# Performance work log

Measured on AMD Instinct MI355X. Metric: run time of the kernel, lower is better.

## Reference

```python
import jax, jax.numpy as jnp
import numpy as np

B, S, D, H = 2, 2048, 1024, 16
DK = D // H  # 64


def setup_inputs() -> dict:
    key = jax.random.key(0)
    ks = jax.random.split(key, 9)
    query = jax.random.normal(ks[0], (B, S, D), dtype=jnp.float32)
    k_in = jax.random.normal(ks[1], (B, S, D), dtype=jnp.float32)
    v_in = jax.random.normal(ks[2], (B, S, D), dtype=jnp.float32)
    mask = jax.random.randint(ks[3], (B, S, S), 0, 2, dtype=jnp.int32)
    sc = 1.0 / np.sqrt(D)
    Wq = jax.random.normal(ks[4], (H, D, DK), dtype=jnp.float32) * sc  # per-head q proj
    Wk = jax.random.normal(ks[5], (H, D, DK), dtype=jnp.float32) * sc
    Wv = jax.random.normal(ks[6], (H, D, DK), dtype=jnp.float32) * sc
    Wu = jax.random.normal(ks[7], (D, D), dtype=jnp.float32) * sc  # unifyheads weight
    bu = jax.random.normal(ks[8], (D,), dtype=jnp.float32) * 0.01
    return {"query": query, "key": k_in, "value": v_in, "mask": mask,
            "Wq": Wq, "Wk": Wk, "Wv": Wv, "Wu": Wu, "bu": bu}


def reference(query, key, value, mask, Wq, Wk, Wv, Wu, bu):
    scale = DK ** 0.25  # original divides q and k each by d_k^(1/4)
    q = jnp.einsum('bsd,hdk->bhsk', query, Wq) / scale
    k = jnp.einsum('bsd,hdk->bhsk', key, Wk) / scale
    v = jnp.einsum('bsd,hdk->bhsk', value, Wv)
    scores = jnp.einsum('bhsk,bhtk->bhst', q, k)  # [B,H,S,S]
    scores = jnp.where(mask[:, None, :, :] == 0, jnp.float32(-1e9), scores)
    attn = jax.nn.softmax(scores, axis=-1)
    out = jnp.einsum('bhst,bhtk->bhsk', attn, v)
    out = jnp.transpose(out, (0, 2, 1, 3)).reshape(query.shape[0], query.shape[1], D)  # concat heads
    return out @ Wu + bu
```

## Files before the change

### kernel.cpp

```cpp
#include <hip/hip_runtime.h>
#include <hip/hip_bf16.h>


typedef __bf16 bf16_t;
typedef __attribute__((ext_vector_type(4))) __bf16 bf16x4;
typedef __attribute__((ext_vector_type(8))) __bf16 bf16x8;
typedef __attribute__((ext_vector_type(4))) float f32x4;
typedef unsigned int u32;

#define B_ 2
#define S_ 2048
#define D_ 1024
#define H_ 16
#define DK_ 64
#define NX_ (4096 * 1024)

static __device__ __forceinline__ f32x4 mfma16(bf16x8 a, bf16x8 b, f32x4 c) {
  return __builtin_amdgcn_mfma_f32_16x16x32_bf16(a, b, c, 0, 0, 0);
}

static __device__ __forceinline__ void async16(const bf16_t* g, bf16_t* l) {
  __builtin_amdgcn_global_load_lds(
      (const __attribute__((address_space(1))) u32*)g,
      (__attribute__((address_space(3))) u32*)l, 16, 0, 0);
}

__global__ __launch_bounds__(256) void cvt_x(const float* __restrict__ q,
                                             const float* __restrict__ k,
                                             const float* __restrict__ v,
                                             bf16_t* __restrict__ qo,
                                             bf16_t* __restrict__ ko,
                                             bf16_t* __restrict__ vo) {
  const int z = blockIdx.y;
  const float* src = (z == 0) ? q : (z == 1) ? k : v;
  bf16_t* dst = (z == 0) ? qo : (z == 1) ? ko : vo;
  size_t i = ((size_t)blockIdx.x * 256 + threadIdx.x) * 8;
  float4 a = *(const float4*)(src + i);
  float4 b = *(const float4*)(src + i + 4);
  bf16x8 o;
  o[0] = (bf16_t)a.x; o[1] = (bf16_t)a.y; o[2] = (bf16_t)a.z; o[3] = (bf16_t)a.w;
  o[4] = (bf16_t)b.x; o[5] = (bf16_t)b.y; o[6] = (bf16_t)b.z; o[7] = (bf16_t)b.w;
  *(bf16x8*)(dst + i) = o;
}

__global__ __launch_bounds__(256) void wtrans(
    const float* __restrict__ Wq, const float* __restrict__ Wk,
    const float* __restrict__ Wv, const float* __restrict__ Wu,
    bf16_t* __restrict__ Bq, bf16_t* __restrict__ Bk,
    bf16_t* __restrict__ Bv, bf16_t* __restrict__ Bu, float qkscale) {
  __shared__ __align__(16) bf16_t T[64][72];
  const int z = blockIdx.z;
  const float* W = (z == 0) ? Wq : (z == 1) ? Wk : (z == 2) ? Wv : Wu;
  bf16_t* BT = (z == 0) ? Bq : (z == 1) ? Bk : (z == 2) ? Bv : Bu;
  const float scale = (z <= 1) ? qkscale : 1.0f;
  const int d0 = blockIdx.x * 64, nt = blockIdx.y;
  const int tid = threadIdx.x;
  const int r = tid & 63, g = tid >> 6;

  const float* src = (z < 3)
      ? W + ((size_t)nt * D_ + d0 + r) * DK_ + g * 16
      : W + (size_t)(d0 + r) * D_ + nt * 64 + g * 16;
#pragma unroll
  for (int j = 0; j < 4; ++j) {
    float4 w4 = *(const float4*)(src + j * 4);
    T[g * 16 + j * 4 + 0][r] = (bf16_t)(w4.x * scale);
    T[g * 16 + j * 4 + 1][r] = (bf16_t)(w4.y * scale);
    T[g * 16 + j * 4 + 2][r] = (bf16_t)(w4.z * scale);
    T[g * 16 + j * 4 + 3][r] = (bf16_t)(w4.w * scale);
  }
  __syncthreads();
  const int orow = tid >> 3, seg = tid & 7;
#pragma unroll
  for (int p = 0; p < 2; ++p) {
    int rr = p * 32 + orow;
    *(bf16x8*)(BT + (size_t)(nt * 64 + rr) * D_ + d0 + seg * 8) =
        *(const bf16x8*)&T[rr][seg * 8];
  }
}

__global__ __launch_bounds__(256) void vt_build(const bf16_t* __restrict__ V,
                                                bf16_t* __restrict__ Vt) {
  __shared__ __align__(16) bf16_t T[64][72];
  const int r0 = blockIdx.x * 64;
  const int c0 = blockIdx.y * 64;
  const int tid = threadIdx.x;
#pragma unroll
  for (int it = 0; it < 2; ++it) {
    int t = tid + it * 256;
    int rr = t >> 3, cc = (t & 7) * 8;
    *(bf16x8*)&T[rr][cc] = *(const bf16x8*)(V + (size_t)(r0 + rr) * D_ + c0 + cc);
  }
  __syncthreads();
#pragma unroll
  for (int it = 0; it < 2; ++it) {
    int t = tid + it * 256;
    int cr = t >> 3, rc = (t & 7) * 8;
    bf16x8 v;
#pragma unroll
    for (int j = 0; j < 8; ++j) v[j] = T[rc + j][cr];
    *(bf16x8*)(Vt + (size_t)(c0 + cr) * 4096 + r0 + rc) = v;
  }
}

__global__ __launch_bounds__(256) void mask_pack(const int* __restrict__ mask,
                                                 unsigned int* __restrict__ bits) {
  int w = blockIdx.x * 256 + threadIdx.x;
  const int4* p = (const int4*)(mask + (size_t)w * 32);
  unsigned int v = 0;
#pragma unroll
  for (int i = 0; i < 8; ++i) {
    int4 m4 = p[i];
    v |= (m4.x != 0 ? 1u : 0u) << (i * 4 + 0);
    v |= (m4.y != 0 ? 1u : 0u) << (i * 4 + 1);
    v |= (m4.z != 0 ? 1u : 0u) << (i * 4 + 2);
    v |= (m4.w != 0 ? 1u : 0u) << (i * 4 + 3);
  }
  bits[w] = v;
}

__global__ __launch_bounds__(256) void gemm_bt(
    const bf16_t* __restrict__ A0, const bf16_t* __restrict__ A1,
    const bf16_t* __restrict__ A2, const bf16_t* __restrict__ BT0,
    const bf16_t* __restrict__ BT1, const bf16_t* __restrict__ BT2,
    bf16_t* __restrict__ C0, bf16_t* __restrict__ C1, bf16_t* __restrict__ C2) {
  __shared__ __align__(16) bf16_t As[128 * 64];
  __shared__ __align__(16) bf16_t Bs[128 * 64];

  const int z = blockIdx.z;
  const bf16_t* A = (z == 0) ? A0 : (z == 1) ? A1 : A2;
  const bf16_t* BT = (z == 0) ? BT0 : (z == 1) ? BT1 : BT2;
  bf16_t* C = (z == 0) ? C0 : (z == 1) ? C1 : C2;

  const int tid = threadIdx.x;
  const int lane = tid & 63, wave = tid >> 6;
  const int l = lane & 15, quad = lane >> 4;
  const int wm = wave >> 1, wn = wave & 1;
  const int row0 = blockIdx.x * 128, col0 = blockIdx.y * 128;

  const int lr = lane >> 3;
  const int gc8 = (lane & 7) ^ lr;
  const int xl = l & 7;

  f32x4 acc[4][4];
#pragma unroll
  for (int i = 0; i < 4; ++i)
#pragma unroll
    for (int j = 0; j < 4; ++j) acc[i][j] = {0.f, 0.f, 0.f, 0.f};

  for (int k0 = 0; k0 < 1024; k0 += 64) {
    __syncthreads();
#pragma unroll
    for (int c = 0; c < 4; ++c) {
      int r = wave * 32 + c * 8;
      async16(A + (size_t)(row0 + r + lr) * 1024 + k0 + gc8 * 8, As + r * 64);
      async16(BT + (size_t)(col0 + r + lr) * 1024 + k0 + gc8 * 8, Bs + r * 64);
    }
    __syncthreads();

#pragma unroll
    for (int kh = 0; kh < 2; ++kh) {
      bf16x8 af[4], bf[4];
#pragma unroll
      for (int f = 0; f < 4; ++f)
        af[f] = *(const bf16x8*)&As[(wm * 64 + f * 16 + l) * 64 +
                                    (((kh * 4 + quad) ^ xl) * 8)];
#pragma unroll
      for (int f = 0; f < 4; ++f)
        bf[f] = *(const bf16x8*)&Bs[(wn * 64 + f * 16 + l) * 64 +
                                    (((kh * 4 + quad) ^ xl) * 8)];
#pragma unroll
      for (int fm = 0; fm < 4; ++fm)
#pragma unroll
        for (int fn = 0; fn < 4; ++fn)
          acc[fm][fn] = mfma16(af[fm], bf[fn], acc[fm][fn]);
    }
  }

#pragma unroll
  for (int fm = 0; fm < 4; ++fm)
#pragma unroll
    for (int fn = 0; fn < 4; ++fn)
#pragma unroll
      for (int reg = 0; reg < 4; ++reg) {
        int row = row0 + wm * 64 + fm * 16 + quad * 4 + reg;
        int col = col0 + wn * 64 + fn * 16 + l;
        C[(size_t)row * 1024 + col] = (bf16_t)acc[fm][fn][reg];
      }
}

__global__ __launch_bounds__(256) void gemm_bt64(
    const bf16_t* __restrict__ A, const bf16_t* __restrict__ BT,
    float* __restrict__ C, const float* __restrict__ bias) {
  __shared__ __align__(16) bf16_t As[64 * 64];
  __shared__ __align__(16) bf16_t Bs[128 * 64];

  const int tid = threadIdx.x;
  const int lane = tid & 63, wave = tid >> 6;
  const int l = lane & 15, quad = lane >> 4;
  const int row0 = blockIdx.x * 64, col0 = blockIdx.y * 128;

  const int lr = lane >> 3;
  const int gc8 = (lane & 7) ^ lr;
  const int xl = l & 7;

  f32x4 acc[4][2];
#pragma unroll
  for (int i = 0; i < 4; ++i)
#pragma unroll
    for (int j = 0; j < 2; ++j) acc[i][j] = {0.f, 0.f, 0.f, 0.f};

  for (int k0 = 0; k0 < 1024; k0 += 64) {
    __syncthreads();
#pragma unroll
    for (int c = 0; c < 2; ++c) {
      int r = wave * 16 + c * 8;
      async16(A + (size_t)(row0 + r + lr) * 1024 + k0 + gc8 * 8, As + r * 64);
    }
#pragma unroll
    for (int c = 0; c < 4; ++c) {
      int r = wave * 32 + c * 8;
      async16(BT + (size_t)(col0 + r + lr) * 1024 + k0 + gc8 * 8, Bs + r * 64);
    }
    __syncthreads();

#pragma unroll
    for (int kh = 0; kh < 2; ++kh) {
      bf16x8 af[4], bf[2];
#pragma unroll
      for (int f = 0; f < 4; ++f)
        af[f] = *(const bf16x8*)&As[(f * 16 + l) * 64 +
                                    (((kh * 4 + quad) ^ xl) * 8)];
#pragma unroll
      for (int f = 0; f < 2; ++f)
        bf[f] = *(const bf16x8*)&Bs[(wave * 32 + f * 16 + l) * 64 +
                                    (((kh * 4 + quad) ^ xl) * 8)];
#pragma unroll
      for (int fm = 0; fm < 4; ++fm)
#pragma unroll
        for (int fn = 0; fn < 2; ++fn)
          acc[fm][fn] = mfma16(af[fm], bf[fn], acc[fm][fn]);
    }
  }

#pragma unroll
  for (int fm = 0; fm < 4; ++fm)
#pragma unroll
    for (int fn = 0; fn < 2; ++fn)
#pragma unroll
      for (int reg = 0; reg < 4; ++reg) {
        int row = row0 + fm * 16 + quad * 4 + reg;
        int col = col0 + wave * 32 + fn * 16 + l;
        C[(size_t)row * 1024 + col] = acc[fm][fn][reg] + bias[col];
      }
}

__global__ __launch_bounds__(256, 4) void attn_kernel(
    const bf16_t* __restrict__ Qx, const bf16_t* __restrict__ Kx,
    const bf16_t* __restrict__ Vt, const unsigned int* __restrict__ mbits,
    bf16_t* __restrict__ out) {
  __shared__ __align__(16) bf16_t Ks[64 * 64];
  __shared__ __align__(16) bf16_t Vts[64 * 64];
  __shared__ __align__(16) bf16_t Ps[4][16][72];

  const int tid = threadIdx.x;
  const int lane = tid & 63, wave = tid >> 6;
  const int l = lane & 15, quad = lane >> 4;
  const int qt = blockIdx.x, h = blockIdx.y, b = blockIdx.z;
  const int ch = h * 64;
  const size_t rb = (size_t)b * S_;
  const int q0 = qt * 64 + wave * 16;

  const int lr = lane >> 3;
  const int gc8 = (lane & 7) ^ lr;
  const int xl = l & 7;

  bf16x8 bq[2];
  {
    const bf16_t* qp = Qx + (rb + q0 + l) * D_ + ch;
    bq[0] = *(const bf16x8*)(qp + quad * 8);
    bq[1] = *(const bf16x8*)(qp + 32 + quad * 8);
  }

  bf16x8 ones;
#pragma unroll
  for (int j = 0; j < 8; ++j) ones[j] = (bf16_t)1.0f;

  const f32x4 zero = {0.f, 0.f, 0.f, 0.f};
  f32x4 o[4];
  f32x4 rs = zero;
#pragma unroll
  for (int nt = 0; nt < 4; ++nt) o[nt] = zero;

  const u32* mrow = mbits + (size_t)(b * S_ + q0 + l) * (S_ / 32);

  for (int t0 = 0; t0 < S_; t0 += 64) {
    __syncthreads();
#pragma unroll
    for (int it = 0; it < 2; ++it) {
      int r0 = it * 32 + wave * 8;
      async16(Kx + (rb + t0 + r0 + lr) * D_ + ch + gc8 * 8, Ks + r0 * 64);
      async16(Vt + (size_t)(ch + r0 + lr) * 4096 + rb + t0 + gc8 * 8,
              Vts + r0 * 64);
    }
    __syncthreads();

    u32 mw0 = mrow[(t0 >> 5)];
    u32 mw1 = mrow[(t0 >> 5) + 1];

#pragma unroll
    for (int ts = 0; ts < 4; ++ts) {
      int rK = (ts * 16 + l) * 64;
      bf16x8 ak0 = *(const bf16x8*)&Ks[rK + ((quad ^ xl) * 8)];
      bf16x8 ak1 = *(const bf16x8*)&Ks[rK + (((4 + quad) ^ xl) * 8)];
      f32x4 s = mfma16(ak0, bq[0], zero);
      s = mfma16(ak1, bq[1], s);

      u32 mw = (ts < 2) ? mw0 : mw1;
      u32 nib = (mw >> ((ts & 1) * 16 + quad * 4)) & 0xFu;
      bf16x4 pv;
#pragma unroll
      for (int reg = 0; reg < 4; ++reg) {
        float e = exp2f(fminf(s[reg], 43.28f));
        int bm = ((int)(nib << (31 - reg))) >> 31;
        float p = __int_as_float(__float_as_int(e) & bm);
        pv[reg] = (bf16_t)p;
      }
      *(bf16x4*)&Ps[wave][l][ts * 16 + quad * 4] = pv;
    }

    bf16x8 ap0 = *(const bf16x8*)&Ps[wave][l][quad * 8];
    bf16x8 ap1 = *(const bf16x8*)&Ps[wave][l][32 + quad * 8];

    __builtin_amdgcn_s_setprio(1);
    rs = mfma16(ap0, ones, rs);
    rs = mfma16(ap1, ones, rs);
#pragma unroll
    for (int nt = 0; nt < 4; ++nt) {
      int rV = (nt * 16 + l) * 64;
      bf16x8 bv0 = *(const bf16x8*)&Vts[rV + ((quad ^ xl) * 8)];
      bf16x8 bv1 = *(const bf16x8*)&Vts[rV + (((4 + quad) ^ xl) * 8)];
      o[nt] = mfma16(ap0, bv0, o[nt]);
      o[nt] = mfma16(ap1, bv1, o[nt]);
    }
    __builtin_amdgcn_s_setprio(0);
  }

#pragma unroll
  for (int reg = 0; reg < 4; ++reg) {
    float inv = (rs[reg] > 0.f) ? (1.f / rs[reg]) : 0.f;
    int srow = q0 + quad * 4 + reg;
    bf16_t* op = out + (rb + srow) * D_ + ch;
#pragma unroll
    for (int nt = 0; nt < 4; ++nt)
      op[nt * 16 + l] = (bf16_t)(o[nt][reg] * inv);
  }
}

extern "C" void kernel_launch(void* const* d_in, const int* in_sizes, int n_in,
                              void* d_out, int out_size, void* d_ws, size_t ws_size,
                              hipStream_t stream) {
  const float* q_in = (const float*)d_in[0];
  const float* k_in = (const float*)d_in[1];
  const float* v_in = (const float*)d_in[2];
  const int* mask = (const int*)d_in[3];
  const float* Wq = (const float*)d_in[4];
  const float* Wk = (const float*)d_in[5];
  const float* Wv = (const float*)d_in[6];
  const float* Wu = (const float*)d_in[7];
  const float* bu = (const float*)d_in[8];
  float* outp = (float*)d_out;

  bf16_t* qx = (bf16_t*)d_ws;
  bf16_t* kx = qx + NX_;
  bf16_t* vx = kx + NX_;
  bf16_t* qb = vx + NX_;
  bf16_t* kb = qb + NX_;
  bf16_t* vb = kb + NX_;
  bf16_t* BTq = vb + NX_;
  bf16_t* BTk = BTq + D_ * D_;
  bf16_t* BTv = BTk + D_ * D_;
  bf16_t* BTu = BTv + D_ * D_;
  unsigned int* mb = (unsigned int*)(BTu + D_ * D_);
  bf16_t* ab = qx;
  bf16_t* vtb = kx;

  const float qkscale = 0.35355339059327373f * 1.2011224087864498f;

  dim3 blk(256);
  cvt_x<<<dim3(2048, 3), blk, 0, stream>>>(q_in, k_in, v_in, qx, kx, vx);
  wtrans<<<dim3(16, 16, 4), blk, 0, stream>>>(Wq, Wk, Wv, Wu, BTq, BTk, BTv, BTu, qkscale);
  mask_pack<<<dim3(1024), blk, 0, stream>>>(mask, mb);
  gemm_bt<<<dim3(32, 8, 3), blk, 0, stream>>>(qx, kx, vx, BTq, BTk, BTv,
                                              qb, kb, vb);
  vt_build<<<dim3(64, 16), blk, 0, stream>>>(vb, vtb);
  attn_kernel<<<dim3(S_ / 64, H_, B_), dim3(256), 0, stream>>>(qb, kb, vtb, mb, ab);
  gemm_bt64<<<dim3(64, 8), blk, 0, stream>>>(ab, BTu, outp, bu);
}
```

Baseline: 285.6 us.

## Double-buffer K/V tiles in attention to overlap async loads with compute

The attention loop now keeps two LDS buffers each for K and V. While the current tile is being computed, it issues the async global-to-LDS load for the next tile and prefetches that tile's mask words. This drops the second barrier per iteration and hides load latency behind the MFMA work. In exchange LDS use doubles and the occupancy hint drops from 4 to 3 blocks. It also removes the clamp before exp2 and extracts mask bits with a single bitfield-extract builtin. Without the clamp, large scores could overflow to infinity.

```diff
diff --git a/kernel.cpp b/kernel.cpp
--- a/kernel.cpp
+++ b/kernel.cpp
@@ -254,12 +254,12 @@
       }
 }
 
-__global__ __launch_bounds__(256, 4) void attn_kernel(
+__global__ __launch_bounds__(256, 3) void attn_kernel(
     const bf16_t* __restrict__ Qx, const bf16_t* __restrict__ Kx,
     const bf16_t* __restrict__ Vt, const unsigned int* __restrict__ mbits,
     bf16_t* __restrict__ out) {
-  __shared__ __align__(16) bf16_t Ks[64 * 64];
-  __shared__ __align__(16) bf16_t Vts[64 * 64];
+  __shared__ __align__(16) bf16_t Ks[2][64 * 64];
+  __shared__ __align__(16) bf16_t Vts[2][64 * 64];
   __shared__ __align__(16) bf16_t Ps[4][16][72];
 
   const int tid = threadIdx.x;
@@ -269,6 +269,7 @@
   const int ch = h * 64;
   const size_t rb = (size_t)b * S_;
   const int q0 = qt * 64 + wave * 16;
+  const int quad4 = quad * 4;
 
   const int lr = lane >> 3;
   const int gc8 = (lane & 7) ^ lr;
@@ -293,39 +294,50 @@
 
   const u32* mrow = mbits + (size_t)(b * S_ + q0 + l) * (S_ / 32);
 
+  auto stage = [&](int t0, int buf) {
+#pragma unroll
+    for (int it = 0; it < 2; ++it) {
+      int r0 = it * 32 + wave * 8;
+      async16(Kx + (rb + t0 + r0 + lr) * D_ + ch + gc8 * 8,
+              &Ks[buf][r0 * 64]);
+      async16(Vt + (size_t)(ch + r0 + lr) * 4096 + rb + t0 + gc8 * 8,
+              &Vts[buf][r0 * 64]);
+    }
+  };
+
+  stage(0, 0);
+  uint2 mwc = *(const uint2*)&mrow[0];
+
+  int cur = 0;
   for (int t0 = 0; t0 < S_; t0 += 64) {
     __syncthreads();
-#pragma unroll
-    for (int it = 0; it < 2; ++it) {
-      int r0 = it * 32 + wave * 8;
-      async16(Kx + (rb + t0 + r0 + lr) * D_ + ch + gc8 * 8, Ks + r0 * 64);
-      async16(Vt + (size_t)(ch + r0 + lr) * 4096 + rb + t0 + gc8 * 8,
-              Vts + r0 * 64);
-    }
-    __syncthreads();
-
-    u32 mw0 = mrow[(t0 >> 5)];
-    u32 mw1 = mrow[(t0 >> 5) + 1];
+    const int tn = t0 + 64;
+    if (tn < S_) stage(tn, cur ^ 1);
+    const int nidx = (tn < S_) ? (tn >> 5) : 0;
+    uint2 mwn = *(const uint2*)&mrow[nidx];
+
+    const bf16_t* Kc = Ks[cur];
+    const bf16_t* Vc = Vts[cur];
 
 #pragma unroll
     for (int ts = 0; ts < 4; ++ts) {
       int rK = (ts * 16 + l) * 64;
-      bf16x8 ak0 = *(const bf16x8*)&Ks[rK + ((quad ^ xl) * 8)];
-      bf16x8 ak1 = *(const bf16x8*)&Ks[rK + (((4 + quad) ^ xl) * 8)];
+      bf16x8 ak0 = *(const bf16x8*)&Kc[rK + ((quad ^ xl) * 8)];
+      bf16x8 ak1 = *(const bf16x8*)&Kc[rK + (((4 + quad) ^ xl) * 8)];
       f32x4 s = mfma16(ak0, bq[0], zero);
       s = mfma16(ak1, bq[1], s);
 
-      u32 mw = (ts < 2) ? mw0 : mw1;
-      u32 nib = (mw >> ((ts & 1) * 16 + quad * 4)) & 0xFu;
+      u32 mw = (ts < 2) ? mwc.x : mwc.y;
+      int base = (ts & 1) * 16 + quad4;
       bf16x4 pv;
 #pragma unroll
       for (int reg = 0; reg < 4; ++reg) {
-        float e = exp2f(fminf(s[reg], 43.28f));
-        int bm = ((int)(nib << (31 - reg))) >> 31;
+        float e = exp2f(s[reg]);
+        int bm = __builtin_amdgcn_sbfe(mw, base + reg, 1);
         float p = __int_as_float(__float_as_int(e) & bm);
         pv[reg] = (bf16_t)p;
       }
-      *(bf16x4*)&Ps[wave][l][ts * 16 + quad * 4] = pv;
+      *(bf16x4*)&Ps[wave][l][ts * 16 + quad4] = pv;
     }
 
     bf16x8 ap0 = *(const bf16x8*)&Ps[wave][l][quad * 8];
@@ -337,18 +349,21 @@
 #pragma unroll
     for (int nt = 0; nt < 4; ++nt) {
       int rV = (nt * 16 + l) * 64;
-      bf16x8 bv0 = *(const bf16x8*)&Vts[rV + ((quad ^ xl) * 8)];
-      bf16x8 bv1 = *(const bf16x8*)&Vts[rV + (((4 + quad) ^ xl) * 8)];
+      bf16x8 bv0 = *(const bf16x8*)&Vc[rV + ((quad ^ xl) * 8)];
+      bf16x8 bv1 = *(const bf16x8*)&Vc[rV + (((4 + quad) ^ xl) * 8)];
       o[nt] = mfma16(ap0, bv0, o[nt]);
       o[nt] = mfma16(ap1, bv1, o[nt]);
     }
     __builtin_amdgcn_s_setprio(0);
+
+    mwc = mwn;
+    cur ^= 1;
   }
 
 #pragma unroll
   for (int reg = 0; reg < 4; ++reg) {
     float inv = (rs[reg] > 0.f) ? (1.f / rs[reg]) : 0.f;
-    int srow = q0 + quad * 4 + reg;
+    int srow = q0 + quad4 + reg;
     bf16_t* op = out + (rb + srow) * D_ + ch;
 #pragma unroll
     for (int nt = 0; nt < 4; ++nt)
```

New measurement: 287.6 us. About the same (+0.7%).
